# Performance work log

Hardware: AMD Instinct MI355X
Metric: run time of the kernel (lower is better)

The kernel has to match this reference:

```python
import jax, jax.numpy as jnp
import numpy as np

EMBED_DIMS = 256

def setup_inputs() -> dict:
    key = jax.random.key(0)
    ks = jax.random.split(key, 6)
    C = EMBED_DIMS
    x = jax.random.normal(ks[0], (4, 2048, C), dtype=jnp.float32)
    prev_x = jax.random.normal(ks[1], (4, 2048, C), dtype=jnp.float32)
    s = 1.0 / np.sqrt(C)
    W_qkv = jax.random.uniform(ks[2], (C, 3 * C), dtype=jnp.float32, minval=-s, maxval=s)
    b_qkv = jax.random.uniform(ks[3], (3 * C,), dtype=jnp.float32, minval=-s, maxval=s)
    W_out = jax.random.uniform(ks[4], (C, C), dtype=jnp.float32, minval=-s, maxval=s)
    b_out = jax.random.uniform(ks[5], (C,), dtype=jnp.float32, minval=-s, maxval=s)
    return {"x": x, "prev_x": prev_x, "W_qkv": W_qkv, "b_qkv": b_qkv,
            "W_out": W_out, "b_out": b_out}

def reference(x, prev_x, W_qkv, b_qkv, W_out, b_out):
    B, N, C = x.shape
    xx = jnp.concatenate([prev_x, x], axis=1)          # [B, S, C], S = 2N
    qkv = xx @ W_qkv + b_qkv                            # [B, S, 3C]
    q, k, v = jnp.split(qkv, 3, axis=-1)                # each [B, S, C]
    scale = 1.0 / jnp.sqrt(jnp.asarray(C, dtype=x.dtype))
    attn = jax.nn.softmax(jnp.einsum('bqc,bkc->bqk', q, k) * scale, axis=-1)
    out = jnp.einsum('bqk,bkc->bqc', attn, v)           # [B, S, C]
    out = out @ W_out + b_out
    return out[:, -N:, :]                               # [B, N, C]
```

## Files before the change

kernel.cpp:

```cpp
#include <hip/hip_runtime.h>

typedef __bf16 bf16;
typedef __attribute__((ext_vector_type(8))) __bf16 bf16x8;
typedef __attribute__((ext_vector_type(4))) __bf16 bf16x4;
typedef __attribute__((ext_vector_type(4))) float f32x4;
typedef __attribute__((ext_vector_type(16))) float f32x16;
typedef __attribute__((ext_vector_type(4))) unsigned u32x4;

#define MFMA16(a, b, c) __builtin_amdgcn_mfma_f32_16x16x32_bf16(a, b, c, 0, 0, 0)
#define MFMA32(a, b, c) __builtin_amdgcn_mfma_f32_32x32x16_bf16(a, b, c, 0, 0, 0)

__device__ inline void gload_lds16(const void* g, void* l) {
  __builtin_amdgcn_global_load_lds(
      (const __attribute__((address_space(1))) void*)g,
      (__attribute__((address_space(3))) void*)l, 16, 0, 0);
}

__device__ inline unsigned packbf(float a, float b) {
  unsigned short x = __builtin_bit_cast(unsigned short, (bf16)a);
  unsigned short y = __builtin_bit_cast(unsigned short, (bf16)b);
  return (unsigned)x | ((unsigned)y << 16);
}

__global__ __launch_bounds__(256) void prep_kernel(
    const float* __restrict__ x, const float* __restrict__ px,
    const float* __restrict__ Wqkv, const float* __restrict__ Wout,
    bf16* __restrict__ Xbf, bf16* __restrict__ Wqkvt, bf16* __restrict__ Woutt)
{
  int tid = blockIdx.x * 256 + threadIdx.x;
  int nth = gridDim.x * 256;
  for (int i = tid; i < (4 * 4096 * 256) / 4; i += nth) {
    int e = i << 2;
    int b = e >> 20;
    int r = e & 1048575;
    const float* src = (r < 524288) ? (px + (b << 19) + r)
                                    : (x + (b << 19) + (r - 524288));
    float4 f = *(const float4*)src;
    bf16x4 o = { (bf16)f.x, (bf16)f.y, (bf16)f.z, (bf16)f.w };
    *(bf16x4*)(Xbf + e) = o;
  }
  for (int i = tid; i < 768 * 256; i += nth) {
    int n = i >> 8, k = i & 255;
    Wqkvt[i] = (bf16)Wqkv[k * 768 + n];
  }
  for (int i = tid; i < 256 * 256; i += nth) {
    int n = i >> 8, k = i & 255;
    Woutt[i] = (bf16)Wout[k * 256 + n];
  }
}

template<int MODE>
__global__ __launch_bounds__(256) void gemm_kernel(
    const bf16* __restrict__ A, const bf16* __restrict__ Wt,
    const float* __restrict__ bias,
    bf16* __restrict__ Qo, bf16* __restrict__ KVo, float* __restrict__ Fo)
{
  const int bm = blockIdx.x * 64;
  const int n0 = blockIdx.y * 128;
  const int tid = threadIdx.x;
  const int lane = tid & 63, w = tid >> 6;
  const int l15 = lane & 15, lg = lane >> 4;

  alignas(16) __shared__ bf16 Alds[64 * 32];
  alignas(16) __shared__ bf16 Wlds[128 * 32];

  f32x4 acc[8] = {};

  for (int k0 = 0; k0 < 256; k0 += 32) {
    __syncthreads();
    {
      int c = tid;
      int row = c >> 2, kc = (c & 3) << 3;
      bf16x8 v = *(const bf16x8*)(A + (size_t)(bm + row) * 256 + k0 + kc);
      *(bf16x8*)((char*)Alds + ((c << 4) ^ (((row >> 1) & 3) << 4))) = v;
    }
    #pragma unroll
    for (int it = 0; it < 2; it++) {
      int c = it * 256 + tid;
      int row = c >> 2, kc = (c & 3) << 3;
      bf16x8 v = *(const bf16x8*)(Wt + (size_t)(n0 + row) * 256 + k0 + kc);
      *(bf16x8*)((char*)Wlds + ((c << 4) ^ (((row >> 1) & 3) << 4))) = v;
    }
    __syncthreads();
    const int arow = w * 16 + l15;
    bf16x8 afr = *(const bf16x8*)((char*)Alds +
        (((arow << 6) + (lg << 4)) ^ (((arow >> 1) & 3) << 4)));
    #pragma unroll
    for (int nt = 0; nt < 8; nt++) {
      const int wrow = nt * 16 + l15;
      bf16x8 bfr = *(const bf16x8*)((char*)Wlds +
          (((wrow << 6) + (lg << 4)) ^ (((wrow >> 1) & 3) << 4)));
      acc[nt] = MFMA16(afr, bfr, acc[nt]);
    }
  }

  #pragma unroll
  for (int nt = 0; nt < 8; nt++) {
    const int n = n0 + nt * 16 + l15;
    const float bv = bias[n];
    const int m0 = bm + w * 16 + lg * 4;
    if (MODE == 0) {
      const int bq = m0 >> 12;
      const int s = m0 & 4095;
      if (n < 256) {
        if (s >= 2048) {
          const int ks = n >> 4, h2 = (n >> 3) & 1, e = n & 7;
          #pragma unroll
          for (int r = 0; r < 4; r++) {
            const int qrow = bq * 2048 + (s - 2048) + r;
            Qo[(size_t)(qrow >> 5) * 8192 + ks * 512 +
               ((qrow & 31) + 32 * h2) * 8 + e] =
                (bf16)((acc[nt][r] + bv) * 0.0625f);
          }
        }
      } else if (n < 512) {
        const int d = n - 256;
        const int ks = d >> 4, h2 = (d >> 3) & 1, e = d & 7;
        const size_t tb = (size_t)(bq * 128 + (s >> 5)) * 16384;
        #pragma unroll
        for (int r = 0; r < 4; r++)
          KVo[tb + ks * 512 + (((s & 31) + r) + 32 * h2) * 8 + e] =
              (bf16)(acc[nt][r] + bv);
      } else {
        const int d = n - 512;
        const int kv32 = s & 31;
        const int sidx = kv32 >> 4, h2 = (kv32 >> 3) & 1, e0 = kv32 & 7;
        bf16x4 st = { (bf16)(acc[nt][0] + bv), (bf16)(acc[nt][1] + bv),
                      (bf16)(acc[nt][2] + bv), (bf16)(acc[nt][3] + bv) };
        *(bf16x4*)(KVo + (size_t)(bq * 128 + (s >> 5)) * 16384 + 8192 +
                   (sidx * 8 + (d >> 5)) * 512 + ((d & 31) + 32 * h2) * 8 + e0) = st;
      }
    } else {
      #pragma unroll
      for (int r = 0; r < 4; r++)
        Fo[(size_t)((m0 + r) * 256 + n)] = acc[nt][r] + bv;
    }
  }
}

__global__ __launch_bounds__(256, 2) void attn_kernel(
    const bf16* __restrict__ Qp, const bf16* __restrict__ KVp,
    bf16* __restrict__ Opart, float* __restrict__ ml)
{
  const int id = blockIdx.x;
  const int c = id & 7;
  const int b = (id >> 3) & 3;
  const int qb = id >> 5;
  const int tid = threadIdx.x;
  const int lane = tid & 63, w = tid >> 6;
  const int l31 = lane & 31, hi = lane >> 5;

  __shared__ bf16 Kb[3][8192];
  __shared__ bf16 Vb[2][8192];

  const int qg = b * 64 + qb * 4 + w;
  const bf16* qbase = Qp + (size_t)qg * 8192 + lane * 8;
  bf16x8 qf[16];
  #pragma unroll
  for (int ks = 0; ks < 16; ks++)
    qf[ks] = *(const bf16x8*)(qbase + ks * 512);

  const char* kvtile0 = (const char*)(KVp + (size_t)(b * 128 + c * 16) * 16384);

  auto stage_K = [&](int t, int ring) {
    const char* g = kvtile0 + (size_t)t * 32768 + w * 4096 + lane * 16;
    char* l = (char*)&Kb[ring][0] + w * 4096;
    #pragma unroll
    for (int j = 0; j < 4; j++)
      gload_lds16(g + j * 1024, l + j * 1024);
  };
  auto stage_V = [&](int t, int ring) {
    const char* g = kvtile0 + (size_t)t * 32768 + 16384 + w * 4096 + lane * 16;
    char* l = (char*)&Vb[ring][0] + w * 4096;
    #pragma unroll
    for (int j = 0; j < 4; j++)
      gload_lds16(g + j * 1024, l + j * 1024);
  };

  auto qk = [&](const bf16* kbuf) {
    f32x16 p = {};
    __builtin_amdgcn_s_setprio(1);
    #pragma unroll
    for (int ks = 0; ks < 16; ks++) {
      bf16x8 kf = *(const bf16x8*)(kbuf + ks * 512 + lane * 8);
      p = MFMA32(kf, qf[ks], p);
    }
    __builtin_amdgcn_s_setprio(0);
    return p;
  };

  stage_K(0, 0);
  stage_V(0, 0);
  stage_K(1, 1);

  f32x16 o[8] = {};
  f32x16 pA;
  float m_run = -1e30f, l_run = 0.f;

  #pragma unroll
  for (int t = 0; t < 16; t++) {
    __syncthreads();
    if (t + 2 < 16) stage_K(t + 2, (t + 2) % 3);
    if (t + 1 < 16) stage_V(t + 1, (t + 1) & 1);

    if (t == 0) pA = qk(&Kb[0][0]);
    f32x16 pN = {};
    if (t + 1 < 16) pN = qk(&Kb[(t + 1) % 3][0]);

    f32x16 p = pA;
    float m0 = fmaxf(p[0], p[1]),   m1 = fmaxf(p[2], p[3]);
    float m2 = fmaxf(p[4], p[5]),   m3 = fmaxf(p[6], p[7]);
    float m4 = fmaxf(p[8], p[9]),   m5 = fmaxf(p[10], p[11]);
    float m6 = fmaxf(p[12], p[13]), m7 = fmaxf(p[14], p[15]);
    m0 = fmaxf(m0, m1); m2 = fmaxf(m2, m3); m4 = fmaxf(m4, m5); m6 = fmaxf(m6, m7);
    float mt = fmaxf(fmaxf(m0, m2), fmaxf(m4, m6));
    mt = fmaxf(mt, __shfl_xor(mt, 32));
    if (!__all(mt <= m_run + 8.f)) {
      const float m_new = fmaxf(m_run, mt);
      const float alpha = __expf(m_run - m_new);
      l_run *= alpha;
      #pragma unroll
      for (int i = 0; i < 8; i++)
        #pragma unroll
        for (int j = 0; j < 16; j++) o[i][j] *= alpha;
      m_run = m_new;
    }
    #pragma unroll
    for (int i = 0; i < 16; i++) p[i] = __expf(p[i] - m_run);
    float s0 = (p[0] + p[1]) + (p[2] + p[3]);
    float s1 = (p[4] + p[5]) + (p[6] + p[7]);
    float s2 = (p[8] + p[9]) + (p[10] + p[11]);
    float s3 = (p[12] + p[13]) + (p[14] + p[15]);
    float ps = (s0 + s1) + (s2 + s3);
    ps += __shfl_xor(ps, 32);
    l_run += ps;

    unsigned u[8], xp[8];
    #pragma unroll
    for (int i = 0; i < 8; i++) u[i] = packbf(p[2 * i], p[2 * i + 1]);
    #pragma unroll
    for (int i = 0; i < 8; i++)
      xp[i] = (unsigned)__shfl_xor((int)u[i], 32);
    const u32x4 w0 = hi ? (u32x4){xp[2], xp[3], u[2], u[3]}
                        : (u32x4){u[0], u[1], xp[0], xp[1]};
    const u32x4 w1 = hi ? (u32x4){xp[6], xp[7], u[6], u[7]}
                        : (u32x4){u[4], u[5], xp[4], xp[5]};
    const bf16x8 pf0 = __builtin_bit_cast(bf16x8, w0);
    const bf16x8 pf1 = __builtin_bit_cast(bf16x8, w1);

    const bf16* vbuf = &Vb[t & 1][0];
    __builtin_amdgcn_s_setprio(1);
    #pragma unroll
    for (int dg = 0; dg < 8; dg++) {
      bf16x8 v0 = *(const bf16x8*)(vbuf + dg * 512 + lane * 8);
      o[dg] = MFMA32(v0, pf0, o[dg]);
      bf16x8 v1 = *(const bf16x8*)(vbuf + (8 + dg) * 512 + lane * 8);
      o[dg] = MFMA32(v1, pf1, o[dg]);
    }
    __builtin_amdgcn_s_setprio(0);

    pA = pN;
  }

  const int q = b * 2048 + qb * 128 + w * 32 + l31;
  bf16* ob = Opart + ((size_t)c * 8192 + q) * 256;
  #pragma unroll
  for (int dg = 0; dg < 8; dg++) {
    #pragma unroll
    for (int r4 = 0; r4 < 4; r4++) {
      const int d = dg * 32 + r4 * 8 + hi * 4;
      bf16x4 st = { (bf16)o[dg][r4 * 4 + 0], (bf16)o[dg][r4 * 4 + 1],
                    (bf16)o[dg][r4 * 4 + 2], (bf16)o[dg][r4 * 4 + 3] };
      *(bf16x4*)(ob + d) = st;
    }
  }
  if (hi == 0) {
    float2 v = { m_run, l_run };
    *(float2*)(ml + ((size_t)c * 8192 + q) * 2) = v;
  }
}

__global__ __launch_bounds__(256) void combine_kernel(
    const bf16* __restrict__ Opart, const float* __restrict__ ml,
    bf16* __restrict__ AO)
{
  const int id = blockIdx.x * 256 + threadIdx.x;
  const int q = id >> 5, dc = (id & 31) << 3;
  float ms[8], ls[8], M = -1e30f;
  #pragma unroll
  for (int s = 0; s < 8; s++) {
    float2 v = *(const float2*)(ml + ((size_t)s * 8192 + q) * 2);
    ms[s] = v.x; ls[s] = v.y;
    M = fmaxf(M, v.x);
  }
  float L = 0.f;
  float acc[8] = {};
  #pragma unroll
  for (int s = 0; s < 8; s++) {
    const float wgt = __expf(ms[s] - M);
    L += ls[s] * wgt;
    bf16x8 v = *(const bf16x8*)(Opart + ((size_t)s * 8192 + q) * 256 + dc);
    #pragma unroll
    for (int j = 0; j < 8; j++) acc[j] += wgt * (float)v[j];
  }
  const float inv = 1.f / L;
  bf16x8 st;
  #pragma unroll
  for (int j = 0; j < 8; j++) st[j] = (bf16)(acc[j] * inv);
  *(bf16x8*)(AO + (size_t)q * 256 + dc) = st;
}

extern "C" void kernel_launch(void* const* d_in, const int* in_sizes, int n_in,
                              void* d_out, int out_size, void* d_ws, size_t ws_size,
                              hipStream_t stream) {
  const float* x    = (const float*)d_in[0];
  const float* px   = (const float*)d_in[1];
  const float* Wqkv = (const float*)d_in[2];
  const float* bqkv = (const float*)d_in[3];
  const float* Wout = (const float*)d_in[4];
  const float* bout = (const float*)d_in[5];
  float* out = (float*)d_out;

  char* ws = (char*)d_ws;
  bf16* Qp    = (bf16*)(ws);
  bf16* KVp   = (bf16*)(ws + 4194304);
  bf16* Woutt = (bf16*)(ws + 20971520);
  bf16* Wqkvt = (bf16*)(ws + 21102592);
  float* ml   = (float*)(ws + 21495808);
  bf16* Xbf   = (bf16*)(ws + 22020096);
  bf16* Opart = (bf16*)(ws + 22020096);
  bf16* AObf  = (bf16*)(ws);

  prep_kernel<<<dim3(512), dim3(256), 0, stream>>>(x, px, Wqkv, Wout,
                                                   Xbf, Wqkvt, Woutt);
  gemm_kernel<0><<<dim3(256, 6), dim3(256), 0, stream>>>(
      Xbf, Wqkvt, bqkv, Qp, KVp, nullptr);
  attn_kernel<<<dim3(512), dim3(256), 0, stream>>>(Qp, KVp, Opart, ml);
  combine_kernel<<<dim3(1024), dim3(256), 0, stream>>>(Opart, ml, AObf);
  gemm_kernel<1><<<dim3(128, 2), dim3(256), 0, stream>>>(
      AObf, Woutt, bout, nullptr, nullptr, out);
}
```

Baseline: 97.63 us.

## Fuse split-KV combine into output projection and load V directly to registers

The separate combine kernel and output-projection GEMM become one out_kernel. It merges the eight partial attention outputs into a swizzled LDS tile and multiplies that tile by W_out in place, which removes the bf16 round trip through global memory and one launch. In the attention kernel, V is no longer staged through LDS. Each wave loads its V fragments straight from global memory into registers, and the K ring drops from triple to double buffering with no QK lookahead. This cuts LDS use and may raise occupancy, but it exposes global-load latency for V and lowers the overlap of QK with softmax.

Result: slower. 124.9 us (+27.9%).

```diff
diff --git a/kernel.cpp b/kernel.cpp
--- a/kernel.cpp
+++ b/kernel.cpp
@@ -49,11 +49,10 @@
   }
 }
 
-template<int MODE>
-__global__ __launch_bounds__(256) void gemm_kernel(
+__global__ __launch_bounds__(256) void gemm_qkv_kernel(
     const bf16* __restrict__ A, const bf16* __restrict__ Wt,
     const float* __restrict__ bias,
-    bf16* __restrict__ Qo, bf16* __restrict__ KVo, float* __restrict__ Fo)
+    bf16* __restrict__ Qo, bf16* __restrict__ KVo)
 {
   const int bm = blockIdx.x * 64;
   const int n0 = blockIdx.y * 128;
@@ -99,41 +98,35 @@
     const int n = n0 + nt * 16 + l15;
     const float bv = bias[n];
     const int m0 = bm + w * 16 + lg * 4;
-    if (MODE == 0) {
-      const int bq = m0 >> 12;
-      const int s = m0 & 4095;
-      if (n < 256) {
-        if (s >= 2048) {
-          const int ks = n >> 4, h2 = (n >> 3) & 1, e = n & 7;
-          #pragma unroll
-          for (int r = 0; r < 4; r++) {
-            const int qrow = bq * 2048 + (s - 2048) + r;
-            Qo[(size_t)(qrow >> 5) * 8192 + ks * 512 +
-               ((qrow & 31) + 32 * h2) * 8 + e] =
-                (bf16)((acc[nt][r] + bv) * 0.0625f);
-          }
+    const int bq = m0 >> 12;
+    const int s = m0 & 4095;
+    if (n < 256) {
+      if (s >= 2048) {
+        const int ks = n >> 4, h2 = (n >> 3) & 1, e = n & 7;
+        #pragma unroll
+        for (int r = 0; r < 4; r++) {
+          const int qrow = bq * 2048 + (s - 2048) + r;
+          Qo[(size_t)(qrow >> 5) * 8192 + ks * 512 +
+             ((qrow & 31) + 32 * h2) * 8 + e] =
+              (bf16)((acc[nt][r] + bv) * 0.0625f);
         }
-      } else if (n < 512) {
-        const int d = n - 256;
-        const int ks = d >> 4, h2 = (d >> 3) & 1, e = d & 7;
-        const size_t tb = (size_t)(bq * 128 + (s >> 5)) * 16384;
-        #pragma unroll
-        for (int r = 0; r < 4; r++)
-          KVo[tb + ks * 512 + (((s & 31) + r) + 32 * h2) * 8 + e] =
-              (bf16)(acc[nt][r] + bv);
-      } else {
-        const int d = n - 512;
-        const int kv32 = s & 31;
-        const int sidx = kv32 >> 4, h2 = (kv32 >> 3) & 1, e0 = kv32 & 7;
-        bf16x4 st = { (bf16)(acc[nt][0] + bv), (bf16)(acc[nt][1] + bv),
-                      (bf16)(acc[nt][2] + bv), (bf16)(acc[nt][3] + bv) };
-        *(bf16x4*)(KVo + (size_t)(bq * 128 + (s >> 5)) * 16384 + 8192 +
-                   (sidx * 8 + (d >> 5)) * 512 + ((d & 31) + 32 * h2) * 8 + e0) = st;
       }
-    } else {
+    } else if (n < 512) {
+      const int d = n - 256;
+      const int ks = d >> 4, h2 = (d >> 3) & 1, e = d & 7;
+      const size_t tb = (size_t)(bq * 128 + (s >> 5)) * 16384;
       #pragma unroll
       for (int r = 0; r < 4; r++)
-        Fo[(size_t)((m0 + r) * 256 + n)] = acc[nt][r] + bv;
+        KVo[tb + ks * 512 + (((s & 31) + r) + 32 * h2) * 8 + e] =
+            (bf16)(acc[nt][r] + bv);
+    } else {
+      const int d = n - 512;
+      const int kv32 = s & 31;
+      const int sidx = kv32 >> 4, h2 = (kv32 >> 3) & 1, e0 = kv32 & 7;
+      bf16x4 st = { (bf16)(acc[nt][0] + bv), (bf16)(acc[nt][1] + bv),
+                    (bf16)(acc[nt][2] + bv), (bf16)(acc[nt][3] + bv) };
+      *(bf16x4*)(KVo + (size_t)(bq * 128 + (s >> 5)) * 16384 + 8192 +
+                 (sidx * 8 + (d >> 5)) * 512 + ((d & 31) + 32 * h2) * 8 + e0) = st;
     }
   }
 }
@@ -150,8 +143,7 @@
   const int lane = tid & 63, w = tid >> 6;
   const int l31 = lane & 31, hi = lane >> 5;
 
-  __shared__ bf16 Kb[3][8192];
-  __shared__ bf16 Vb[2][8192];
+  __shared__ bf16 Kb[2][8192];
 
   const int qg = b * 64 + qb * 4 + w;
   const bf16* qbase = Qp + (size_t)qg * 8192 + lane * 8;
@@ -162,22 +154,31 @@
 
   const char* kvtile0 = (const char*)(KVp + (size_t)(b * 128 + c * 16) * 16384);
 
-  auto stage_K = [&](int t, int ring) {
+  auto stage_K = [&](int t) {
     const char* g = kvtile0 + (size_t)t * 32768 + w * 4096 + lane * 16;
-    char* l = (char*)&Kb[ring][0] + w * 4096;
+    char* l = (char*)&Kb[t & 1][0] + w * 4096;
     #pragma unroll
     for (int j = 0; j < 4; j++)
       gload_lds16(g + j * 1024, l + j * 1024);
   };
-  auto stage_V = [&](int t, int ring) {
-    const char* g = kvtile0 + (size_t)t * 32768 + 16384 + w * 4096 + lane * 16;
-    char* l = (char*)&Vb[ring][0] + w * 4096;
-    #pragma unroll
-    for (int j = 0; j < 4; j++)
-      gload_lds16(g + j * 1024, l + j * 1024);
-  };
-
-  auto qk = [&](const bf16* kbuf) {
+
+  stage_K(0);
+
+  f32x16 o[8] = {};
+  float m_run = -1e30f, l_run = 0.f;
+
+  #pragma unroll
+  for (int t = 0; t < 16; t++) {
+    __syncthreads();
+    if (t + 1 < 16) stage_K(t + 1);
+
+    const char* vg = kvtile0 + (size_t)t * 32768 + 16384 + lane * 16;
+    bf16x8 vrA[8];
+    #pragma unroll
+    for (int j = 0; j < 8; j++)
+      vrA[j] = *(const bf16x8*)(vg + j * 1024);
+
+    const bf16* kbuf = &Kb[t & 1][0];
     f32x16 p = {};
     __builtin_amdgcn_s_setprio(1);
     #pragma unroll
@@ -186,28 +187,12 @@
       p = MFMA32(kf, qf[ks], p);
     }
     __builtin_amdgcn_s_setprio(0);
-    return p;
-  };
-
-  stage_K(0, 0);
-  stage_V(0, 0);
-  stage_K(1, 1);
-
-  f32x16 o[8] = {};
-  f32x16 pA;
-  float m_run = -1e30f, l_run = 0.f;
-
-  #pragma unroll
-  for (int t = 0; t < 16; t++) {
-    __syncthreads();
-    if (t + 2 < 16) stage_K(t + 2, (t + 2) % 3);
-    if (t + 1 < 16) stage_V(t + 1, (t + 1) & 1);
-
-    if (t == 0) pA = qk(&Kb[0][0]);
-    f32x16 pN = {};
-    if (t + 1 < 16) pN = qk(&Kb[(t + 1) % 3][0]);
-
-    f32x16 p = pA;
+
+    bf16x8 vrB[8];
+    #pragma unroll
+    for (int j = 0; j < 8; j++)
+      vrB[j] = *(const bf16x8*)(vg + (8 + j) * 1024);
+
     float m0 = fmaxf(p[0], p[1]),   m1 = fmaxf(p[2], p[3]);
     float m2 = fmaxf(p[4], p[5]),   m3 = fmaxf(p[6], p[7]);
     float m4 = fmaxf(p[8], p[9]),   m5 = fmaxf(p[10], p[11]);
@@ -248,18 +233,13 @@
     const bf16x8 pf0 = __builtin_bit_cast(bf16x8, w0);
     const bf16x8 pf1 = __builtin_bit_cast(bf16x8, w1);
 
-    const bf16* vbuf = &Vb[t & 1][0];
     __builtin_amdgcn_s_setprio(1);
     #pragma unroll
     for (int dg = 0; dg < 8; dg++) {
-      bf16x8 v0 = *(const bf16x8*)(vbuf + dg * 512 + lane * 8);
-      o[dg] = MFMA32(v0, pf0, o[dg]);
-      bf16x8 v1 = *(const bf16x8*)(vbuf + (8 + dg) * 512 + lane * 8);
-      o[dg] = MFMA32(v1, pf1, o[dg]);
+      o[dg] = MFMA32(vrA[dg], pf0, o[dg]);
+      o[dg] = MFMA32(vrB[dg], pf1, o[dg]);
     }
     __builtin_amdgcn_s_setprio(0);
-
-    pA = pN;
   }
 
   const int q = b * 2048 + qb * 128 + w * 32 + l31;
@@ -280,34 +260,80 @@
   }
 }
 
-__global__ __launch_bounds__(256) void combine_kernel(
+__global__ __launch_bounds__(256) void out_kernel(
     const bf16* __restrict__ Opart, const float* __restrict__ ml,
-    bf16* __restrict__ AO)
+    const bf16* __restrict__ Woutt, const float* __restrict__ bout,
+    float* __restrict__ out)
 {
-  const int id = blockIdx.x * 256 + threadIdx.x;
-  const int q = id >> 5, dc = (id & 31) << 3;
-  float ms[8], ls[8], M = -1e30f;
-  #pragma unroll
-  for (int s = 0; s < 8; s++) {
-    float2 v = *(const float2*)(ml + ((size_t)s * 8192 + q) * 2);
-    ms[s] = v.x; ls[s] = v.y;
-    M = fmaxf(M, v.x);
-  }
-  float L = 0.f;
-  float acc[8] = {};
-  #pragma unroll
-  for (int s = 0; s < 8; s++) {
-    const float wgt = __expf(ms[s] - M);
-    L += ls[s] * wgt;
-    bf16x8 v = *(const bf16x8*)(Opart + ((size_t)s * 8192 + q) * 256 + dc);
-    #pragma unroll
-    for (int j = 0; j < 8; j++) acc[j] += wgt * (float)v[j];
-  }
-  const float inv = 1.f / L;
-  bf16x8 st;
-  #pragma unroll
-  for (int j = 0; j < 8; j++) st[j] = (bf16)(acc[j] * inv);
-  *(bf16x8*)(AO + (size_t)q * 256 + dc) = st;
+  const int bm = blockIdx.x * 32;
+  const int tid = threadIdx.x;
+  const int lane = tid & 63, w = tid >> 6;
+  const int l15 = lane & 15, lg = lane >> 4;
+
+  alignas(16) __shared__ bf16 Alds[32 * 256];
+  alignas(16) __shared__ bf16 Wlds[256 * 32];
+
+  #pragma unroll
+  for (int ch = 0; ch < 4; ch++) {
+    const int idx = ch * 256 + tid;
+    const int row = idx >> 5;
+    const int dc = (idx & 31) << 3;
+    const int q = bm + row;
+    float ms[8], ls[8], M = -1e30f;
+    #pragma unroll
+    for (int s = 0; s < 8; s++) {
+      float2 v = *(const float2*)(ml + ((size_t)s * 8192 + q) * 2);
+      ms[s] = v.x; ls[s] = v.y;
+      M = fmaxf(M, v.x);
+    }
+    float L = 0.f, acc[8] = {};
+    #pragma unroll
+    for (int s = 0; s < 8; s++) {
+      const float wgt = __expf(ms[s] - M);
+      L += ls[s] * wgt;
+      bf16x8 v = *(const bf16x8*)(Opart + ((size_t)s * 8192 + q) * 256 + dc);
+      #pragma unroll
+      for (int j = 0; j < 8; j++) acc[j] += wgt * (float)v[j];
+    }
+    const float inv = 1.f / L;
+    bf16x8 st;
+    #pragma unroll
+    for (int j = 0; j < 8; j++) st[j] = (bf16)(acc[j] * inv);
+    *(bf16x8*)((char*)Alds + ((row * 512 + dc * 2) ^ ((row & 7) << 4))) = st;
+  }
+
+  f32x4 acc[8] = {};
+  for (int k0 = 0; k0 < 8; k0++) {
+    __syncthreads();
+    #pragma unroll
+    for (int it = 0; it < 4; it++) {
+      int cidx = it * 256 + tid;
+      int row = cidx >> 2, kc = (cidx & 3) << 3;
+      bf16x8 v = *(const bf16x8*)(Woutt + (size_t)row * 256 + k0 * 32 + kc);
+      *(bf16x8*)((char*)Wlds + ((cidx << 4) ^ (((row >> 1) & 3) << 4))) = v;
+    }
+    __syncthreads();
+    const int arow = (w & 1) * 16 + l15;
+    bf16x8 afr = *(const bf16x8*)((char*)Alds +
+        ((arow * 512 + k0 * 64 + lg * 16) ^ ((arow & 7) << 4)));
+    #pragma unroll
+    for (int nt = 0; nt < 8; nt++) {
+      const int wrow = (w >> 1) * 128 + nt * 16 + l15;
+      bf16x8 bfr = *(const bf16x8*)((char*)Wlds +
+          (((wrow << 6) + (lg << 4)) ^ (((wrow >> 1) & 3) << 4)));
+      acc[nt] = MFMA16(afr, bfr, acc[nt]);
+    }
+  }
+
+  #pragma unroll
+  for (int nt = 0; nt < 8; nt++) {
+    const int n = (w >> 1) * 128 + nt * 16 + l15;
+    const float bvv = bout[n];
+    const int m0 = bm + (w & 1) * 16 + lg * 4;
+    #pragma unroll
+    for (int r = 0; r < 4; r++)
+      out[(size_t)(m0 + r) * 256 + n] = acc[nt][r] + bvv;
+  }
 }
 
 extern "C" void kernel_launch(void* const* d_in, const int* in_sizes, int n_in,
@@ -329,14 +355,11 @@
   float* ml   = (float*)(ws + 21495808);
   bf16* Xbf   = (bf16*)(ws + 22020096);
   bf16* Opart = (bf16*)(ws + 22020096);
-  bf16* AObf  = (bf16*)(ws);
 
   prep_kernel<<<dim3(512), dim3(256), 0, stream>>>(x, px, Wqkv, Wout,
                                                    Xbf, Wqkvt, Woutt);
-  gemm_kernel<0><<<dim3(256, 6), dim3(256), 0, stream>>>(
-      Xbf, Wqkvt, bqkv, Qp, KVp, nullptr);
+  gemm_qkv_kernel<<<dim3(256, 6), dim3(256), 0, stream>>>(
+      Xbf, Wqkvt, bqkv, Qp, KVp);
   attn_kernel<<<dim3(512), dim3(256), 0, stream>>>(Qp, KVp, Opart, ml);
-  combine_kernel<<<dim3(1024), dim3(256), 0, stream>>>(Opart, ml, AObf);
-  gemm_kernel<1><<<dim3(128, 2), dim3(256), 0, stream>>>(
-      AObf, Woutt, bout, nullptr, nullptr, out);
-}
+  out_kernel<<<dim3(256), dim3(256), 0, stream>>>(Opart, ml, Woutt, bout, out);
+}
```
